# Kernel tuning notes

Measured on AMD Instinct MI355X. Metric: run time of the kernel, lower is better.

Reference implementation:

```python
import jax, jax.numpy as jnp
import numpy as np

TOKENS = 1024
HIDDEN = 1024
INTER = 4096
N_EXPERTS = 8


def setup_inputs() -> dict:
    key = jax.random.key(0)
    k1, k2, k3, k4 = jax.random.split(key, 4)
    hidden_states = jax.random.normal(k1, (TOKENS, HIDDEN), dtype=jnp.float32)
    # multi-hot expert assignment mask [tokens, num_experts] with values in {0,1}
    expert_indices = jax.random.randint(k2, (TOKENS, N_EXPERTS), 0, 2, dtype=jnp.int32)
    # Phi3MLP weights per expert (Linear layers have bias=False in Phi3)
    scale_gu = 1.0 / np.sqrt(HIDDEN)
    scale_d = 1.0 / np.sqrt(INTER)
    w_gate_up = jax.random.normal(k3, (N_EXPERTS, HIDDEN, 2 * INTER), dtype=jnp.float32) * scale_gu
    w_down = jax.random.normal(k4, (N_EXPERTS, INTER, HIDDEN), dtype=jnp.float32) * scale_d
    return {
        "hidden_states": hidden_states,
        "expert_indices": expert_indices,
        "w_gate_up": w_gate_up,
        "w_down": w_down,
    }


def reference(hidden_states, expert_indices, w_gate_up, w_down):
    # Original loops per expert: gather masked tokens, run Phi3MLP, scatter-add back.
    # Mathematically equivalent dense form (jit-friendly, static shapes):
    #   out = sum_e mask[:, e] * Phi3MLP_e(x)
    # gate_up: [E, T, 2*I]
    gu = jnp.einsum('th,ehi->eti', hidden_states, w_gate_up)
    gate, up = jnp.split(gu, 2, axis=-1)  # each [E, T, I]
    act = up * jax.nn.silu(gate)          # Phi3MLP: up * silu(gate)
    y = jnp.einsum('eti,eih->eth', act, w_down)  # [E, T, H]
    mask = expert_indices.astype(hidden_states.dtype)  # [T, E]
    out = jnp.einsum('eth,te->th', y, mask)
    return out
```

## Files before the change

kernel.cpp:

```cpp
#include <hip/hip_runtime.h>
#include <hip/hip_bf16.h>
#include <stdint.h>

#define T_TOK 1024
#define HID   1024
#define INT_  4096
#define NE    8

typedef __attribute__((ext_vector_type(4))) float f32x4;
typedef __attribute__((ext_vector_type(8))) short short8;

__device__ int g_tok[NE][T_TOK];
__device__ int g_cnt[NE];

__device__ __forceinline__ uint32_t pack2bf(float a, float b) {
  unsigned short ua = __builtin_bit_cast(unsigned short, (__bf16)a);
  unsigned short ub = __builtin_bit_cast(unsigned short, (__bf16)b);
  return (uint32_t)ua | ((uint32_t)ub << 16);
}

#define GL16(gsrc, ldst)                                                       \
  __builtin_amdgcn_global_load_lds(                                            \
      (const __attribute__((address_space(1))) void*)(gsrc),                   \
      (__attribute__((address_space(3))) void*)(ldst), 16, 0, 0)

__global__ void k0_compact(const int* __restrict__ mask)
{
  const int w    = threadIdx.x >> 6;
  const int lane = threadIdx.x & 63;
  if (w >= NE) return;
  const unsigned long long ltmask = (1ull << lane) - 1ull;
  int base = 0;
  #pragma unroll
  for (int c = 0; c < T_TOK / 64; ++c) {
    const int t = c * 64 + lane;
    const bool pred = mask[t * NE + w] != 0;
    const unsigned long long bal = __ballot(pred);
    if (pred) g_tok[w][base + __popcll(bal & ltmask)] = t;
    base += __popcll(bal);
  }
  if (lane == 0) g_cnt[w] = base;
}

__global__ void cvt_x(const float* __restrict__ xin, unsigned short* __restrict__ xout)
{
  const int i = (blockIdx.x * 256 + threadIdx.x) * 8;
  f32x4 a = *(const f32x4*)(xin + i);
  f32x4 b = *(const f32x4*)(xin + i + 4);
  uint4 u;
  u.x = pack2bf(a[0], a[1]); u.y = pack2bf(a[2], a[3]);
  u.z = pack2bf(b[0], b[1]); u.w = pack2bf(b[2], b[3]);
  *(uint4*)(xout + i) = u;
}

__global__ void cvt_T(const float* __restrict__ in, unsigned short* __restrict__ out,
                      int R, int C)
{
  __shared__ float tile[64][65];
  const int e  = blockIdx.z;
  const int c0 = blockIdx.x * 64;
  const int r0 = blockIdx.y * 64;
  const float*    ip = in  + (size_t)e * R * C;
  unsigned short* op = out + (size_t)e * R * C;
  const int t  = threadIdx.x;
  const int rr = t >> 4, c4 = (t & 15) * 4;
  #pragma unroll
  for (int s = 0; s < 4; ++s) {
    f32x4 v = *(const f32x4*)(ip + (size_t)(r0 + s * 16 + rr) * C + c0 + c4);
    tile[s * 16 + rr][c4 + 0] = v[0];
    tile[s * 16 + rr][c4 + 1] = v[1];
    tile[s * 16 + rr][c4 + 2] = v[2];
    tile[s * 16 + rr][c4 + 3] = v[3];
  }
  __syncthreads();
  const int c = t >> 2, rs = (t & 3) * 16;
  uint4 u0, u1;
  u0.x = pack2bf(tile[rs + 0][c],  tile[rs + 1][c]);
  u0.y = pack2bf(tile[rs + 2][c],  tile[rs + 3][c]);
  u0.z = pack2bf(tile[rs + 4][c],  tile[rs + 5][c]);
  u0.w = pack2bf(tile[rs + 6][c],  tile[rs + 7][c]);
  u1.x = pack2bf(tile[rs + 8][c],  tile[rs + 9][c]);
  u1.y = pack2bf(tile[rs + 10][c], tile[rs + 11][c]);
  u1.z = pack2bf(tile[rs + 12][c], tile[rs + 13][c]);
  u1.w = pack2bf(tile[rs + 14][c], tile[rs + 15][c]);
  unsigned short* orow = op + (size_t)(c0 + c) * R + r0 + rs;
  *(uint4*)(orow)     = u0;
  *(uint4*)(orow + 8) = u1;
}

__global__ __launch_bounds__(512, 1)
void k1_gateup(const unsigned short* __restrict__ xb,
               const unsigned short* __restrict__ wguT,
               unsigned short* __restrict__ act)
{
  const int e   = blockIdx.z;
  const int cnt = g_cnt[e];
  const int mt  = blockIdx.y;
  const int t0  = mt * 256;
  if (t0 >= cnt) return;

  __shared__ char sA [2][256 * 128];
  __shared__ char sBg[2][128 * 128];
  __shared__ char sBu[2][128 * 128];

  const int nt   = blockIdx.x;
  const int tid  = threadIdx.x;
  const int lane = tid & 63;
  const int wv   = tid >> 6;
  const int wm   = (wv >> 2) * 128;
  const int wn   = (wv & 3) * 32;
  const int n0   = nt * 128;

  const unsigned short* wg = wguT + (size_t)e * 8192 * HID + (size_t)n0 * HID;
  const unsigned short* wu = wg + (size_t)4096 * HID;

  f32x4 accg[8][2], accu[8][2];
  #pragma unroll
  for (int i = 0; i < 8; ++i)
    #pragma unroll
    for (int j = 0; j < 2; ++j) {
      accg[i][j] = (f32x4){0.f, 0.f, 0.f, 0.f};
      accu[i][j] = (f32x4){0.f, 0.f, 0.f, 0.f};
    }

  const int drow  = lane >> 3;
  const int dchk8 = (((lane & 7) ^ drow) << 3);

  int tokA[4];
  #pragma unroll
  for (int s = 0; s < 4; ++s)
    tokA[s] = g_tok[e][t0 + (s * 8 + wv) * 8 + drow];

#define K1_STAGE(B, KT)                                                        \
  do {                                                                         \
    _Pragma("unroll")                                                          \
    for (int s_ = 0; s_ < 4; ++s_) {                                           \
      const int rb_ = (s_ * 8 + wv) * 8;                                       \
      GL16(xb + (size_t)tokA[s_] * HID + (KT) + dchk8, sA[B] + rb_ * 128);     \
    }                                                                          \
    _Pragma("unroll")                                                          \
    for (int s_ = 0; s_ < 2; ++s_) {                                           \
      const int rb_ = (s_ * 8 + wv) * 8;                                       \
      GL16(wg + (size_t)(rb_ + drow) * HID + (KT) + dchk8, sBg[B] + rb_ * 128);\
      GL16(wu + (size_t)(rb_ + drow) * HID + (KT) + dchk8, sBu[B] + rb_ * 128);\
    }                                                                          \
  } while (0)

  K1_STAGE(0, 0);
  __syncthreads();

  #pragma unroll 2
  for (int t = 0; t < 16; ++t) {
    const int cur = t & 1;
    if (t < 15) K1_STAGE((t + 1) & 1, (t + 1) * 64);
    #pragma unroll
    for (int ks = 0; ks < 2; ++ks) {
      const int kfb = ks * 64 + ((lane >> 4) << 4);
      short8 af[8], bg[2], bu[2];
      #pragma unroll
      for (int i = 0; i < 8; ++i) {
        const int r = wm + i * 16 + (lane & 15);
        af[i] = *(const short8*)(sA[cur] + r * 128 + (kfb ^ ((r & 7) << 4)));
      }
      #pragma unroll
      for (int j = 0; j < 2; ++j) {
        const int r = wn + j * 16 + (lane & 15);
        const int off = r * 128 + (kfb ^ ((r & 7) << 4));
        bg[j] = *(const short8*)(sBg[cur] + off);
        bu[j] = *(const short8*)(sBu[cur] + off);
      }
      #pragma unroll
      for (int i = 0; i < 8; ++i)
        #pragma unroll
        for (int j = 0; j < 2; ++j) {
          accg[i][j] = __builtin_amdgcn_mfma_f32_16x16x32_bf16(af[i], bg[j], accg[i][j], 0, 0, 0);
          accu[i][j] = __builtin_amdgcn_mfma_f32_16x16x32_bf16(af[i], bu[j], accu[i][j], 0, 0, 0);
        }
    }
    __syncthreads();
  }
#undef K1_STAGE

  unsigned short* ab = act + (size_t)e * T_TOK * INT_;
  #pragma unroll
  for (int i = 0; i < 8; ++i) {
    #pragma unroll
    for (int r = 0; r < 4; ++r) {
      const int slot = t0 + wm + i * 16 + ((lane >> 4) << 2) + r;
      if (slot < cnt) {
        #pragma unroll
        for (int j = 0; j < 2; ++j) {
          const int col = n0 + wn + j * 16 + (lane & 15);
          const float g = accg[i][j][r];
          const float u = accu[i][j][r];
          const float s = u * g / (1.f + __expf(-g));
          ab[(size_t)slot * INT_ + col] = __builtin_bit_cast(unsigned short, (__bf16)s);
        }
      }
    }
  }
}

__global__ __launch_bounds__(256, 2)
void k2_down(const unsigned short* __restrict__ act,
             const unsigned short* __restrict__ wdT,
             float* __restrict__ out)
{
  const int e   = blockIdx.z;
  const int cnt = g_cnt[e];
  const int mt  = blockIdx.y >> 2;
  const int ks4 = blockIdx.y & 3;
  const int t0  = mt * 128;
  if (t0 >= cnt) return;

  __shared__ char sA[2][128 * 128];
  __shared__ char sB[2][128 * 128];

  const int nt   = blockIdx.x;
  const int tid  = threadIdx.x;
  const int lane = tid & 63;
  const int wv   = tid >> 6;
  const int wm   = (wv >> 1) * 64;
  const int wn   = (wv & 1) * 64;
  const int n0   = nt * 128;

  const unsigned short* ab = act + (size_t)e * T_TOK * INT_;
  const unsigned short* wb = wdT + (size_t)e * HID * INT_ + (size_t)n0 * INT_;

  f32x4 acc[4][4];
  #pragma unroll
  for (int i = 0; i < 4; ++i)
    #pragma unroll
    for (int j = 0; j < 4; ++j) acc[i][j] = (f32x4){0.f, 0.f, 0.f, 0.f};

  const int drow  = lane >> 3;
  const int dchk8 = (((lane & 7) ^ drow) << 3);
  const int kbeg  = ks4 * (INT_ / 4);

#define K2_STAGE(B, KT)                                                        \
  do {                                                                         \
    _Pragma("unroll")                                                          \
    for (int s_ = 0; s_ < 4; ++s_) {                                           \
      const int rb_ = (s_ * 4 + wv) * 8;                                       \
      GL16(ab + (size_t)(t0 + rb_ + drow) * INT_ + (KT) + dchk8, sA[B] + rb_ * 128); \
      GL16(wb + (size_t)(rb_ + drow) * INT_ + (KT) + dchk8, sB[B] + rb_ * 128);      \
    }                                                                          \
  } while (0)

  K2_STAGE(0, kbeg);
  __syncthreads();

  #pragma unroll 2
  for (int t = 0; t < 16; ++t) {
    const int cur = t & 1;
    if (t < 15) K2_STAGE((t + 1) & 1, kbeg + (t + 1) * 64);
    #pragma unroll
    for (int ks = 0; ks < 2; ++ks) {
      const int kfb = ks * 64 + ((lane >> 4) << 4);
      short8 af[4], bf[4];
      #pragma unroll
      for (int i = 0; i < 4; ++i) {
        const int r = wm + i * 16 + (lane & 15);
        af[i] = *(const short8*)(sA[cur] + r * 128 + (kfb ^ ((r & 7) << 4)));
      }
      #pragma unroll
      for (int j = 0; j < 4; ++j) {
        const int r = wn + j * 16 + (lane & 15);
        bf[j] = *(const short8*)(sB[cur] + r * 128 + (kfb ^ ((r & 7) << 4)));
      }
      #pragma unroll
      for (int i = 0; i < 4; ++i)
        #pragma unroll
        for (int j = 0; j < 4; ++j)
          acc[i][j] = __builtin_amdgcn_mfma_f32_16x16x32_bf16(af[i], bf[j], acc[i][j], 0, 0, 0);
    }
    __syncthreads();
  }
#undef K2_STAGE

  #pragma unroll
  for (int i = 0; i < 4; ++i) {
    #pragma unroll
    for (int r = 0; r < 4; ++r) {
      const int slot = t0 + wm + i * 16 + ((lane >> 4) << 2) + r;
      if (slot < cnt) {
        const int token = g_tok[e][slot];
        #pragma unroll
        for (int j = 0; j < 4; ++j) {
          const int col = n0 + wn + j * 16 + (lane & 15);
          atomicAdd(out + (size_t)token * HID + col, acc[i][j][r]);
        }
      }
    }
  }
}

extern "C" void kernel_launch(void* const* d_in, const int* in_sizes, int n_in,
                              void* d_out, int out_size, void* d_ws, size_t ws_size,
                              hipStream_t stream) {
  const float* x   = (const float*)d_in[0];
  const int*   idx = (const int*)d_in[1];
  const float* wgu = (const float*)d_in[2];
  const float* wd  = (const float*)d_in[3];
  float* out = (float*)d_out;

  char* ws = (char*)d_ws;
  unsigned short* act  = (unsigned short*)(ws);
  unsigned short* xb16 = (unsigned short*)(ws + 67108864);
  unsigned short* wguT = (unsigned short*)(ws + 69206016);
  unsigned short* wdT  = (unsigned short*)(ws + 203423744);

  hipMemsetAsync(d_out, 0, (size_t)out_size * sizeof(float), stream);

  k0_compact<<<1, 512, 0, stream>>>(idx);
  cvt_x<<<T_TOK * HID / (256 * 8), 256, 0, stream>>>(x, xb16);
  cvt_T<<<dim3(8192 / 64, 1024 / 64, NE), 256, 0, stream>>>(wgu, wguT, 1024, 8192);
  cvt_T<<<dim3(1024 / 64, 4096 / 64, NE), 256, 0, stream>>>(wd, wdT, 4096, 1024);

  dim3 g1(INT_ / 128, T_TOK / 256, NE);
  k1_gateup<<<g1, dim3(512), 0, stream>>>(xb16, wguT, act);

  dim3 g2(HID / 128, (T_TOK / 128) * 4, NE);
  k2_down<<<g2, dim3(256), 0, stream>>>(act, wdT, out);
}
```

Baseline: 362.7 us.

## Triple-buffer gate-up GEMM with explicit vmcnt waits and halve N tile

The gate-up kernel now uses a three-stage LDS ring with prefetch two tiles ahead, explicit s_waitcnt vmcnt counts and raw s_barrier in place of __syncthreads. Its N tile shrinks from 128 to 64, which halves per-wave accumulators and doubles the grid. The down kernel gets the same explicit vmcnt/barrier treatment with its double buffer. The aim is to keep more global loads in flight and avoid full waitcnt drains at each barrier. In exchange, the smaller N tile reloads the gathered A tile more often, and the hand-counted vmcnt values depend on the exact number of loads issued per stage.

```diff
diff --git a/kernel.cpp b/kernel.cpp
--- a/kernel.cpp
+++ b/kernel.cpp
@@ -99,24 +99,24 @@
   const int t0  = mt * 256;
   if (t0 >= cnt) return;
 
-  __shared__ char sA [2][256 * 128];
-  __shared__ char sBg[2][128 * 128];
-  __shared__ char sBu[2][128 * 128];
+  __shared__ char sA [3][256 * 128];
+  __shared__ char sBg[3][64 * 128];
+  __shared__ char sBu[3][64 * 128];
 
   const int nt   = blockIdx.x;
   const int tid  = threadIdx.x;
   const int lane = tid & 63;
   const int wv   = tid >> 6;
-  const int wm   = (wv >> 2) * 128;
-  const int wn   = (wv & 3) * 32;
-  const int n0   = nt * 128;
+  const int wm   = (wv >> 1) * 64;
+  const int wn   = (wv & 1) * 32;
+  const int n0   = nt * 64;
 
   const unsigned short* wg = wguT + (size_t)e * 8192 * HID + (size_t)n0 * HID;
   const unsigned short* wu = wg + (size_t)4096 * HID;
 
-  f32x4 accg[8][2], accu[8][2];
-  #pragma unroll
-  for (int i = 0; i < 8; ++i)
+  f32x4 accg[4][2], accu[4][2];
+  #pragma unroll
+  for (int i = 0; i < 4; ++i)
     #pragma unroll
     for (int j = 0; j < 2; ++j) {
       accg[i][j] = (f32x4){0.f, 0.f, 0.f, 0.f};
@@ -131,59 +131,66 @@
   for (int s = 0; s < 4; ++s)
     tokA[s] = g_tok[e][t0 + (s * 8 + wv) * 8 + drow];
 
-#define K1_STAGE(B, KT)                                                        \
+#define K1_STAGE(B, T_)                                                        \
   do {                                                                         \
+    const int kt_ = (T_) * 64;                                                 \
     _Pragma("unroll")                                                          \
     for (int s_ = 0; s_ < 4; ++s_) {                                           \
       const int rb_ = (s_ * 8 + wv) * 8;                                       \
-      GL16(xb + (size_t)tokA[s_] * HID + (KT) + dchk8, sA[B] + rb_ * 128);     \
+      GL16(xb + (size_t)tokA[s_] * HID + kt_ + dchk8, sA[B] + rb_ * 128);      \
     }                                                                          \
-    _Pragma("unroll")                                                          \
-    for (int s_ = 0; s_ < 2; ++s_) {                                           \
-      const int rb_ = (s_ * 8 + wv) * 8;                                       \
-      GL16(wg + (size_t)(rb_ + drow) * HID + (KT) + dchk8, sBg[B] + rb_ * 128);\
-      GL16(wu + (size_t)(rb_ + drow) * HID + (KT) + dchk8, sBu[B] + rb_ * 128);\
+    {                                                                          \
+      const int rb_ = wv * 8;                                                  \
+      GL16(wg + (size_t)(rb_ + drow) * HID + kt_ + dchk8, sBg[B] + rb_ * 128); \
+      GL16(wu + (size_t)(rb_ + drow) * HID + kt_ + dchk8, sBu[B] + rb_ * 128); \
     }                                                                          \
   } while (0)
 
   K1_STAGE(0, 0);
-  __syncthreads();
-
-  #pragma unroll 2
+  K1_STAGE(1, 1);
+
+  #pragma unroll
   for (int t = 0; t < 16; ++t) {
-    const int cur = t & 1;
-    if (t < 15) K1_STAGE((t + 1) & 1, (t + 1) * 64);
+    if (t + 2 < 16) K1_STAGE((t + 2) % 3, t + 2);
+    if (t < 14)      asm volatile("s_waitcnt vmcnt(12)" ::: "memory");
+    else if (t == 14) asm volatile("s_waitcnt vmcnt(6)" ::: "memory");
+    else              asm volatile("s_waitcnt vmcnt(0)" ::: "memory");
+    __builtin_amdgcn_s_barrier();
+    __builtin_amdgcn_sched_barrier(0);
+    const char* cA  = sA [t % 3];
+    const char* cBg = sBg[t % 3];
+    const char* cBu = sBu[t % 3];
     #pragma unroll
     for (int ks = 0; ks < 2; ++ks) {
       const int kfb = ks * 64 + ((lane >> 4) << 4);
-      short8 af[8], bg[2], bu[2];
-      #pragma unroll
-      for (int i = 0; i < 8; ++i) {
+      short8 af[4], bg[2], bu[2];
+      #pragma unroll
+      for (int i = 0; i < 4; ++i) {
         const int r = wm + i * 16 + (lane & 15);
-        af[i] = *(const short8*)(sA[cur] + r * 128 + (kfb ^ ((r & 7) << 4)));
+        af[i] = *(const short8*)(cA + r * 128 + (kfb ^ ((r & 7) << 4)));
       }
       #pragma unroll
       for (int j = 0; j < 2; ++j) {
         const int r = wn + j * 16 + (lane & 15);
         const int off = r * 128 + (kfb ^ ((r & 7) << 4));
-        bg[j] = *(const short8*)(sBg[cur] + off);
-        bu[j] = *(const short8*)(sBu[cur] + off);
-      }
-      #pragma unroll
-      for (int i = 0; i < 8; ++i)
+        bg[j] = *(const short8*)(cBg + off);
+        bu[j] = *(const short8*)(cBu + off);
+      }
+      #pragma unroll
+      for (int i = 0; i < 4; ++i)
         #pragma unroll
         for (int j = 0; j < 2; ++j) {
           accg[i][j] = __builtin_amdgcn_mfma_f32_16x16x32_bf16(af[i], bg[j], accg[i][j], 0, 0, 0);
           accu[i][j] = __builtin_amdgcn_mfma_f32_16x16x32_bf16(af[i], bu[j], accu[i][j], 0, 0, 0);
         }
     }
-    __syncthreads();
+    __builtin_amdgcn_s_barrier();
   }
 #undef K1_STAGE
 
   unsigned short* ab = act + (size_t)e * T_TOK * INT_;
   #pragma unroll
-  for (int i = 0; i < 8; ++i) {
+  for (int i = 0; i < 4; ++i) {
     #pragma unroll
     for (int r = 0; r < 4; ++r) {
       const int slot = t0 + wm + i * 16 + ((lane >> 4) << 2) + r;
@@ -248,12 +255,15 @@
   } while (0)
 
   K2_STAGE(0, kbeg);
-  __syncthreads();
-
-  #pragma unroll 2
+
+  #pragma unroll
   for (int t = 0; t < 16; ++t) {
     const int cur = t & 1;
-    if (t < 15) K2_STAGE((t + 1) & 1, kbeg + (t + 1) * 64);
+    if (t < 15) K2_STAGE(cur ^ 1, kbeg + (t + 1) * 64);
+    if (t < 15) asm volatile("s_waitcnt vmcnt(8)" ::: "memory");
+    else        asm volatile("s_waitcnt vmcnt(0)" ::: "memory");
+    __builtin_amdgcn_s_barrier();
+    __builtin_amdgcn_sched_barrier(0);
     #pragma unroll
     for (int ks = 0; ks < 2; ++ks) {
       const int kfb = ks * 64 + ((lane >> 4) << 4);
@@ -274,7 +284,7 @@
         for (int j = 0; j < 4; ++j)
           acc[i][j] = __builtin_amdgcn_mfma_f32_16x16x32_bf16(af[i], bf[j], acc[i][j], 0, 0, 0);
     }
-    __syncthreads();
+    __builtin_amdgcn_s_barrier();
   }
 #undef K2_STAGE
 
@@ -317,7 +327,7 @@
   cvt_T<<<dim3(8192 / 64, 1024 / 64, NE), 256, 0, stream>>>(wgu, wguT, 1024, 8192);
   cvt_T<<<dim3(1024 / 64, 4096 / 64, NE), 256, 0, stream>>>(wd, wdT, 4096, 1024);
 
-  dim3 g1(INT_ / 128, T_TOK / 256, NE);
+  dim3 g1(INT_ / 64, T_TOK / 256, NE);
   k1_gateup<<<g1, dim3(512), 0, stream>>>(xb16, wguT, act);
 
   dim3 g2(HID / 128, (T_TOK / 128) * 4, NE);
```

Result: faster. 346.1 us (-4.6%).
